# Kernel tuning notes

Measured on AMD Instinct MI355X. Metric: run time of the kernel, lower is better.

## Reference

```python
import jax, jax.numpy as jnp
import numpy as np

B_, N_, D_ = 8, 1024, 64
H_, DH_ = 4, 16
DI_, DS_, DTR_ = 128, 64, 4
MAXP = 512


def _ln(x, w, b, eps=1e-5):
    m = jnp.mean(x, -1, keepdims=True)
    v = jnp.mean((x - m) ** 2, -1, keepdims=True)
    return (x - m) * jax.lax.rsqrt(v + eps) * w + b


def _attn(x, drop_mask, Wq, Wkv, Wo, bo, rel_emb):
    b, n, d = x.shape
    scale = DH_ ** -0.5
    q = (x @ Wq).reshape(b, n, H_, DH_).transpose(0, 2, 1, 3)
    kv = x @ Wkv
    k = kv[..., :d].reshape(b, n, H_, DH_).transpose(0, 2, 1, 3)
    v = kv[..., d:].reshape(b, n, H_, DH_).transpose(0, 2, 1, 3)
    dots = jnp.einsum('bhid,bhjd->bhij', q, k) * scale
    seq = jnp.arange(n)
    dist = jnp.clip(seq[:, None] - seq[None, :], -MAXP, MAXP) + MAXP
    rpe = rel_emb[dist]  # (n, n, DH_)
    dots = dots + jnp.einsum('bhid,ijd->bhij', q, rpe) * scale
    # stochastic key drop: Bernoulli(0.3) positions get -1e12
    dots = dots + drop_mask.astype(dots.dtype) * (-1e12)
    attn = jax.nn.softmax(dots, axis=-1)
    out = jnp.einsum('bhij,bhjd->bhid', attn, v)
    out = out.transpose(0, 2, 1, 3).reshape(b, n, H_ * DH_)
    return out @ Wo + bo


def _mamba(x, W_in, conv_w, conv_b, W_xproj, W_dt, b_dt, A_log, Dm, W_out):
    b, n, _ = x.shape
    xz = x @ W_in                      # (b, n, 2*DI_)
    u, z = xz[..., :DI_], xz[..., DI_:]
    uc = u.transpose(0, 2, 1)          # (b, DI_, n)
    uc = jax.lax.conv_general_dilated(
        uc, conv_w[:, None, :], (1,), ((3, 0),),
        feature_group_count=DI_, dimension_numbers=('NCH', 'OIH', 'NCH'))
    uc = uc + conv_b[None, :, None]
    u = jax.nn.silu(uc).transpose(0, 2, 1)  # (b, n, DI_)
    xdb = u @ W_xproj                  # (b, n, DTR_+2*DS_)
    dt = jax.nn.softplus(xdb[..., :DTR_] @ W_dt + b_dt)  # (b, n, DI_)
    Bm = xdb[..., DTR_:DTR_ + DS_]
    Cm = xdb[..., DTR_ + DS_:]
    A = -jnp.exp(A_log)                # (DI_, DS_)

    def step(h, inp):
        dt_t, B_t, C_t, u_t = inp      # (b,DI_),(b,DS_),(b,DS_),(b,DI_)
        dA = jnp.exp(dt_t[..., None] * A)
        h = h * dA + (dt_t * u_t)[..., None] * B_t[:, None, :]
        y = jnp.einsum('bds,bs->bd', h, C_t)
        return h, y

    h0 = jnp.zeros((b, DI_, DS_), x.dtype)
    xs = (dt.transpose(1, 0, 2), Bm.transpose(1, 0, 2),
          Cm.transpose(1, 0, 2), u.transpose(1, 0, 2))
    _, ys = jax.lax.scan(step, h0, xs)
    y = ys.transpose(1, 0, 2) + u * Dm
    y = y * jax.nn.silu(z)
    return y @ W_out


def _rmsgn(x, gamma, eps=1e-5, groups=4):
    shp = x.shape
    dpg = shp[-1] // groups
    xg = x.reshape(shp[:-1] + (groups, dpg))
    rms = jnp.sqrt(jnp.sum(xg * xg, -1, keepdims=True)) * (dpg ** -0.5)
    return (xg / (rms + eps)).reshape(shp) * gamma


def _ff1(x, c1_w, c1_b, d1_w, d1_b):
    # SwiGLUConvDeconv1d(64, 256, kernel=4, shift=1); x: (b, s2, 64)
    s2 = x.shape[1]
    xc = x.transpose(0, 2, 1)
    xc = jnp.pad(xc, ((0, 0), (0, 0), (3, 3)))
    xc = jax.lax.conv_general_dilated(
        xc, c1_w, (1,), 'VALID', dimension_numbers=('NCH', 'OIH', 'NCH'))
    xc = xc + c1_b[None, :, None]
    gate = jax.nn.silu(xc[:, 256:, :])
    xc = xc[:, :256, :] * gate
    # ConvTranspose1d stride 1 == conv with flipped kernel, full padding
    w = jnp.flip(d1_w, -1).transpose(1, 0, 2)  # (64, 256, 4)
    xc = jax.lax.conv_general_dilated(
        xc, w, (1,), ((3, 3),), dimension_numbers=('NCH', 'OIH', 'NCH'))
    xc = xc + d1_b[None, :, None]
    out = xc.transpose(0, 2, 1)
    return out[:, 3:3 + s2, :]


def _forward(x, drop_mask, ln1_w, ln1_b, Wq, Wkv, Wo, bo, rel_emb,
             ln2_w, ln2_b, W_in, conv_w, conv_b, W_xproj, W_dt, b_dt,
             A_log, Dm, W_out, gamma, c1_w, c1_b, d1_w, d1_b, ln3_w, ln3_b):
    xt = _ln(x, ln1_w, ln1_b)
    xt = _attn(xt, drop_mask, Wq, Wkv, Wo, bo, rel_emb) + x
    x = x + xt  # dropout p=0 -> identity (faithful to original residual math)
    xt = _ln(x, ln2_w, ln2_b)
    m = _mamba(xt, W_in, conv_w, conv_b, W_xproj, W_dt, b_dt, A_log, Dm, W_out)
    m = jnp.where(m >= 0, m, 0.01 * m)  # leaky_relu
    m = _rmsgn(m, gamma)
    m = m + 0.5 * _ff1(m, c1_w, c1_b, d1_w, d1_b)
    x = x + m
    return _ln(x, ln3_w, ln3_b)


def setup_inputs() -> dict:
    ks = jax.random.split(jax.random.key(0), 16)
    g = lambda i, shp, s: jax.random.normal(ks[i], shp, dtype=jnp.float32) * s
    A_log = jnp.log(jnp.tile(jnp.arange(1, DS_ + 1, dtype=jnp.float32)[None, :], (DI_, 1)))
    return {
        'x': jax.random.normal(ks[0], (B_, N_, D_), dtype=jnp.float32),
        'drop_mask': jax.random.bernoulli(ks[1], 0.3, (B_, H_, N_, N_)),
        'ln1_w': jnp.ones((D_,), jnp.float32), 'ln1_b': jnp.zeros((D_,), jnp.float32),
        'Wq': g(2, (D_, D_), 0.1), 'Wkv': g(3, (D_, 2 * D_), 0.1),
        'Wo': g(4, (D_, D_), 0.1), 'bo': jnp.zeros((D_,), jnp.float32),
        'rel_emb': g(5, (2 * MAXP + 1, DH_), 0.02),
        'ln2_w': jnp.ones((D_,), jnp.float32), 'ln2_b': jnp.zeros((D_,), jnp.float32),
        'W_in': g(6, (D_, 2 * DI_), 0.1),
        'conv_w': g(7, (DI_, 4), 0.2), 'conv_b': jnp.zeros((DI_,), jnp.float32),
        'W_xproj': g(8, (DI_, DTR_ + 2 * DS_), 0.1),
        'W_dt': g(9, (DTR_, DI_), 0.1), 'b_dt': jnp.zeros((DI_,), jnp.float32),
        'A_log': A_log, 'Dm': jnp.ones((DI_,), jnp.float32),
        'W_out': g(10, (DI_, D_), 0.1),
        'gamma': jnp.ones((D_,), jnp.float32),
        'c1_w': g(11, (512, 64, 4), 0.1), 'c1_b': jnp.zeros((512,), jnp.float32),
        'd1_w': g(12, (256, 64, 4), 0.1), 'd1_b': jnp.zeros((64,), jnp.float32),
        'ln3_w': jnp.ones((D_,), jnp.float32), 'ln3_b': jnp.zeros((D_,), jnp.float32),
    }


def reference(x, drop_mask, ln1_w, ln1_b, Wq, Wkv, Wo, bo, rel_emb,
              ln2_w, ln2_b, W_in, conv_w, conv_b, W_xproj, W_dt, b_dt,
              A_log, Dm, W_out, gamma, c1_w, c1_b, d1_w, d1_b, ln3_w, ln3_b):
    return _forward(x, drop_mask, ln1_w, ln1_b, Wq, Wkv, Wo, bo, rel_emb,
                    ln2_w, ln2_b, W_in, conv_w, conv_b, W_xproj, W_dt, b_dt,
                    A_log, Dm, W_out, gamma, c1_w, c1_b, d1_w, d1_b, ln3_w, ln3_b)
```

## Files before the change

kernel.cpp:

```cpp
#include <hip/hip_runtime.h>
#include <math.h>


__device__ __forceinline__ float wsum64(float v){
#pragma unroll
  for(int m=32;m>0;m>>=1) v += __shfl_xor(v, m, 64);
  return v;
}
__device__ __forceinline__ float wmax64(float v){
#pragma unroll
  for(int m=32;m>0;m>>=1) v = fmaxf(v, __shfl_xor(v, m, 64));
  return v;
}
__device__ __forceinline__ float silu_f(float x){ return x / (1.f + __expf(-x)); }

__global__ __launch_bounds__(256) void k_ln1_qkv(
    const float* __restrict__ x, const float* __restrict__ w1, const float* __restrict__ b1,
    const float* __restrict__ Wq, const float* __restrict__ Wkv,
    const float* __restrict__ rel, const float* __restrict__ c1w,
    float* __restrict__ qb, float2* __restrict__ kvT,
    float* __restrict__ relT, float* __restrict__ c1wT){
  int lane = threadIdx.x & 63, warp = threadIdx.x >> 6;
  int token = blockIdx.x*4 + warp;
  __shared__ float xt[4][64];
  float xv = x[(size_t)token*64 + lane];
  float mean = wsum64(xv) * 0.015625f;
  float dlt = xv - mean;
  float var = wsum64(dlt*dlt) * 0.015625f;
  float xn = dlt * rsqrtf(var + 1e-5f) * w1[lane] + b1[lane];
  xt[warp][lane] = xn;
  __syncthreads();
  float aq=0.f, ak=0.f, av=0.f;
#pragma unroll 4
  for(int dd=0; dd<64; ++dd){
    float xd = xt[warp][dd];
    aq += xd * Wq[dd*64 + lane];
    ak += xd * Wkv[dd*128 + lane];
    av += xd * Wkv[dd*128 + 64 + lane];
  }
  int b = token >> 10, i = token & 1023;
  int h = lane >> 4, dh = lane & 15;
  size_t o  = (((size_t)(b*4 + h))*1024 + i)*16 + dh;
  size_t oT = (((size_t)(b*4 + h))*16 + dh)*1024 + i;
  qb[o]=aq;
  kvT[oT] = make_float2(ak, av);

  if (blockIdx.x < 65){
    int idx = blockIdx.x*256 + threadIdx.x;
    if (idx < 16*1025){
      int c = idx / 1025;
      int d = idx - c*1025;
      relT[idx] = rel[d*16 + c];
    }
  } else if (blockIdx.x < 577){
    int idx = (blockIdx.x-65)*256 + threadIdx.x;
    int row = idx >> 9;
    int ii  = idx & 511;
    c1wT[idx] = c1w[(size_t)ii*256 + row];
  }
}

__global__ __launch_bounds__(256) void k_kmax(
    const float2* __restrict__ kvT, float* __restrict__ Kmax){
  int bh = blockIdx.x; int tid = threadIdx.x;
  const float2* base = kvT + (size_t)bh*16*1024;
  float mx = 0.f;
#pragma unroll
  for(int r=0;r<4;++r){
    int j = tid + 256*r;
    float ss = 0.f;
#pragma unroll
    for(int c=0;c<16;++c){ float2 kv = base[c*1024 + j]; ss += kv.x*kv.x; }
    mx = fmaxf(mx, ss);
  }
  mx = wmax64(mx);
  __shared__ float red[4];
  int lane = tid&63, wv = tid>>6;
  if(lane==0) red[wv]=mx;
  __syncthreads();
  if(tid==0) Kmax[bh] = sqrtf(fmaxf(fmaxf(red[0],red[1]),fmaxf(red[2],red[3])));
}

__global__ __launch_bounds__(256, 3) void k_attn(
    const float* __restrict__ qb, const float2* __restrict__ kvT,
    const int* __restrict__ dmask, const float* __restrict__ relT,
    const float* __restrict__ Kmax, float* __restrict__ attn_raw){
  int tid = threadIdx.x;
  int lane = tid & 63, wv = tid >> 6;
  int bh  = blockIdx.y;
  int i0  = blockIdx.x*8;
  int b = bh >> 2, h = bh & 3;
  int r0 = wv*2, r1 = wv*2 + 1;

  __shared__ float Gc[8][1024];
  __shared__ float qs[8][16];
  __shared__ float G0s[8], G1024s[8];
  __shared__ float gmS[8];
  __shared__ float Ms[8];
  __shared__ float sums[8];

  if (tid < 128){
    int r = tid >> 4, c = tid & 15;
    qs[r][c] = qb[((size_t)bh*1024 + i0 + r)*16 + c] * 0.25f;
  }
  __syncthreads();

#pragma unroll 1
  for(int bb=0; bb<5; ++bb){
    int d = tid + 256*bb;
    if (d <= 1024){
      float rl[16];
#pragma unroll
      for(int c=0;c<16;++c) rl[c] = relT[c*1025 + d];
#pragma unroll
      for(int r=0;r<8;++r){
        float g = 0.f;
#pragma unroll
        for(int c=0;c<16;++c) g += qs[r][c]*rl[c];
        if (d == 0)        G0s[r] = g;
        else if (d == 1024) G1024s[r] = g;
        else {
          int j = i0 + r + 512 - d;
          if (j >= 0 && j < 1024) Gc[r][j] = g;
        }
      }
    }
  }
  __syncthreads();
#pragma unroll
  for(int r=0;r<8;++r){
    float g0 = G0s[r], g1 = G1024s[r];
    int lo = i0 + r - 512;
    int hi = i0 + r + 512;
#pragma unroll
    for(int p=0;p<4;++p){
      int j = tid + 256*p;
      if (j >= hi) Gc[r][j] = g0;
      else if (j <= lo) Gc[r][j] = g1;
    }
  }
  __syncthreads();
  {
    int r = tid >> 5, jb = tid & 31;
    float gm = -3.0e38f;
#pragma unroll
    for(int k=0;k<32;++k) gm = fmaxf(gm, Gc[r][jb + 32*k]);
#pragma unroll
    for(int m=1;m<32;m<<=1) gm = fmaxf(gm, __shfl_xor(gm, m, 64));
    if ((lane&31)==0) gmS[r] = gm;
  }
  __syncthreads();
  if (tid < 8){
    float qn = 0.f;
#pragma unroll
    for(int c=0;c<16;++c) qn += qs[tid][c]*qs[tid][c];
    Ms[tid] = gmS[tid] + sqrtf(qn)*Kmax[bh];
  }
  __syncthreads();

  float q0[16], q1[16];
#pragma unroll
  for(int c=0;c<16;++c){ q0[c]=qs[r0][c]; q1[c]=qs[r1][c]; }
  float M0 = Ms[r0], M1 = Ms[r1];

  const float2* kvb = kvT + (size_t)bh*16*1024;
  const int* mb0 = dmask + ((size_t)bh*1024 + i0 + r0)*1024;
  const int* mb1 = dmask + ((size_t)bh*1024 + i0 + r1)*1024;

  float s0=0.f, s1=0.f;
  float a0[16], a1[16];
#pragma unroll
  for(int c=0;c<16;++c){ a0[c]=0.f; a1[c]=0.f; }

#pragma unroll 1
  for(int t=0;t<16;++t){
    int j = lane + 64*t;
    int mk0 = mb0[j], mk1 = mb1[j];
    float2 kv[16];
#pragma unroll
    for(int c=0;c<16;++c) kv[c] = kvb[c*1024 + j];
    float sv0 = Gc[r0][j], sv1 = Gc[r1][j];
#pragma unroll
    for(int c=0;c<16;++c){ sv0 += q0[c]*kv[c].x; sv1 += q1[c]*kv[c].x; }
    float p0 = mk0 ? 0.f : __expf(sv0 - M0);
    float p1 = mk1 ? 0.f : __expf(sv1 - M1);
    s0 += p0; s1 += p1;
#pragma unroll
    for(int c=0;c<16;++c){ a0[c] += p0*kv[c].y; a1[c] += p1*kv[c].y; }
  }
  s0 = wsum64(s0); s1 = wsum64(s1);
#pragma unroll
  for(int c=0;c<16;++c){
    float x0 = a0[c];
    x0 += __shfl_xor(x0, 32, 64); x0 += __shfl_xor(x0, 16, 64);
    a0[c] = x0;
    float x1 = a1[c];
    x1 += __shfl_xor(x1, 32, 64); x1 += __shfl_xor(x1, 16, 64);
    a1[c] = x1;
  }
  __syncthreads();
  float* red = &Gc[0][0];
  if (lane < 16){
#pragma unroll
    for(int c=0;c<16;++c){
      red[r0*272 + lane*17 + c] = a0[c];
      red[r1*272 + lane*17 + c] = a1[c];
    }
  }
  if (lane == 0){ sums[r0] = s0; sums[r1] = s1; }
  __syncthreads();
  if (tid < 128){
    int row = tid >> 4, c = tid & 15;
    float tot = 0.f;
#pragma unroll
    for(int g=0; g<16; ++g) tot += red[row*272 + g*17 + c];
    attn_raw[((size_t)b*1024 + i0 + row)*64 + h*16 + c] = tot / sums[row];
  }
}

__global__ __launch_bounds__(256) void k_post_attn(
    const float* __restrict__ x, const float* __restrict__ attn_raw,
    const float* __restrict__ Wo, const float* __restrict__ bo,
    const float* __restrict__ ln2w, const float* __restrict__ ln2b,
    const float* __restrict__ W_in,
    float* __restrict__ x2, float* __restrict__ u0, float* __restrict__ zsarr){
  int tid = threadIdx.x;
  int lane = tid & 63, wv = tid >> 6;
  int tok0 = blockIdx.x * 16;
  __shared__ float arS[16][64];
  __shared__ float lnS[16][64];
  for(int l = tid; l < 1024; l += 256)
    arS[l >> 6][l & 63] = attn_raw[(size_t)tok0*64 + l];
  __syncthreads();
#pragma unroll 1
  for(int tt = 0; tt < 4; ++tt){
    int tl = wv*4 + tt;
    int token = tok0 + tl;
    float acc = bo[lane];
#pragma unroll 4
    for(int dd = 0; dd < 64; ++dd) acc += arS[tl][dd] * Wo[dd*64 + lane];
    float t = 2.f*x[(size_t)token*64 + lane] + acc;
    x2[(size_t)token*64 + lane] = t;
    float mean = wsum64(t)*0.015625f;
    float dlt = t - mean;
    float var = wsum64(dlt*dlt)*0.015625f;
    lnS[tl][lane] = dlt*rsqrtf(var+1e-5f)*ln2w[lane] + ln2b[lane];
  }
  __syncthreads();
  int oc = tid;
  float w[64];
#pragma unroll
  for(int dd = 0; dd < 64; ++dd) w[dd] = W_in[dd*256 + oc];
  const float4* lnS4 = (const float4*)&lnS[0][0];
#pragma unroll 1
  for(int tl = 0; tl < 16; ++tl){
    float acc = 0.f;
#pragma unroll
    for(int d4 = 0; d4 < 16; ++d4){
      float4 l4 = lnS4[tl*16 + d4];
      acc += l4.x*w[4*d4] + l4.y*w[4*d4+1] + l4.z*w[4*d4+2] + l4.w*w[4*d4+3];
    }
    int token = tok0 + tl;
    if (oc < 128) u0[(size_t)token*128 + oc] = acc;
    else          zsarr[(size_t)token*128 + (oc-128)] = silu_f(acc);
  }
}

__global__ __launch_bounds__(256) void k_conv_proj(
    const float* __restrict__ u0, const float* __restrict__ conv_w, const float* __restrict__ conv_b,
    const float* __restrict__ W_xproj, const float* __restrict__ W_dt, const float* __restrict__ b_dt,
    float* __restrict__ uarr, float* __restrict__ Bmp, float* __restrict__ Cmp, float* __restrict__ dtarr){
  int sub = threadIdx.x >> 7, c = threadIdx.x & 127;
  int token = blockIdx.x*2 + sub;
  int b = token >> 10, i = token & 1023;
  __shared__ float us[2][128];
  __shared__ float dtin[2][4];
  float acc = conv_b[c];
#pragma unroll
  for(int k2=0;k2<4;++k2){
    int t2 = i - 3 + k2;
    if (t2 >= 0) acc += u0[((size_t)b*1024 + t2)*128 + c]*conv_w[c*4+k2];
  }
  float uv = silu_f(acc);
  uarr[(size_t)token*128 + c] = uv;
  us[sub][c] = uv;
  __syncthreads();
  float accA = 0.f, accB = 0.f;
  int cB = 128 + (c & 3);
#pragma unroll 4
  for(int dd=0; dd<128; ++dd){
    float xd = us[sub][dd];
    accA += xd * W_xproj[dd*132 + c];
    accB += xd * W_xproj[dd*132 + cB];
  }
  if (c < 4){ dtin[sub][c] = accA; Cmp[(size_t)token*64 + 60 + c] = accB; }
  else if (c < 68) Bmp[(size_t)token*64 + (c-4)] = accA;
  else             Cmp[(size_t)token*64 + (c-68)] = accA;
  __syncthreads();
  float dv = b_dt[c];
#pragma unroll
  for(int r2=0;r2<4;++r2) dv += dtin[sub][r2]*W_dt[r2*128 + c];
  dv = fmaxf(dv, 0.f) + log1pf(expf(-fabsf(dv)));
  dtarr[(size_t)token*128 + c] = dv;
}

__global__ __launch_bounds__(256) void k_scan_a(
    const float* __restrict__ dtarr, const float* __restrict__ uarr,
    const float* __restrict__ Bmp, const float* __restrict__ A_log,
    float* __restrict__ Parr, float* __restrict__ Rarr){
  int lane = threadIdx.x & 63, warp = threadIdx.x >> 6;
  int w = blockIdx.x*4 + warp;
  int c = w & 7, d = (w >> 3) & 127, b = w >> 10;
  float A = -expf(A_log[d*64 + lane]);
  int tb = c*128;
  const float* dtp = dtarr + ((size_t)b*1024 + tb)*128 + d;
  const float* up  = uarr  + ((size_t)b*1024 + tb)*128 + d;
  const float* Bp  = Bmp   + ((size_t)b*1024 + tb)*64 + lane;
  float R = 0.f, sdt = 0.f;
  for(int t0=0; t0<128; t0+=8){
    float dtc[8], uc[8], Bc[8];
#pragma unroll
    for(int r=0;r<8;++r){
      dtc[r]=dtp[(size_t)(t0+r)*128]; uc[r]=up[(size_t)(t0+r)*128]; Bc[r]=Bp[(size_t)(t0+r)*64];
    }
#pragma unroll
    for(int r=0;r<8;++r){
      float dt = dtc[r];
      R = R*__expf(dt*A) + dt*uc[r]*Bc[r];
      sdt += dt;
    }
  }
  Parr[(size_t)w*64 + lane] = __expf(sdt*A);
  Rarr[(size_t)w*64 + lane] = R;
}

__global__ __launch_bounds__(256) void k_scan_c(
    const float* __restrict__ dtarr, const float* __restrict__ uarr,
    const float* __restrict__ Bmp, const float* __restrict__ Cmp,
    const float* __restrict__ zsarr, const float* __restrict__ A_log,
    const float* __restrict__ Dm, const float* __restrict__ Parr,
    const float* __restrict__ Rarr, float* __restrict__ ymp){
  int lane = threadIdx.x & 63, warp = threadIdx.x >> 6;
  int w = blockIdx.x*4 + warp;
  int c = w & 7, d = (w >> 3) & 127, b = w >> 10;
  float A = -expf(A_log[d*64 + lane]);
  float Dv = Dm[d];
  float h = 0.f;
  int wbase = w - c;
#pragma unroll 1
  for(int cp=0; cp<c; ++cp){
    float P = Parr[(size_t)(wbase+cp)*64 + lane];
    float R = Rarr[(size_t)(wbase+cp)*64 + lane];
    h = h*P + R;
  }
  int tb = c*128;
  const float* dtp = dtarr + ((size_t)b*1024 + tb)*128 + d;
  const float* up  = uarr  + ((size_t)b*1024 + tb)*128 + d;
  const float* zp  = zsarr + ((size_t)b*1024 + tb)*128 + d;
  const float* Bp  = Bmp   + ((size_t)b*1024 + tb)*64 + lane;
  const float* Cp  = Cmp   + ((size_t)b*1024 + tb)*64 + lane;
  float* yp        = ymp   + ((size_t)b*1024 + tb)*128 + d;
  for(int t0=0; t0<128; t0+=8){
    float dtc[8], uc[8], Bc[8], Cc[8], zc[8];
#pragma unroll
    for(int r=0;r<8;++r){
      dtc[r]=dtp[(size_t)(t0+r)*128]; uc[r]=up[(size_t)(t0+r)*128];
      Bc[r]=Bp[(size_t)(t0+r)*64];    Cc[r]=Cp[(size_t)(t0+r)*64];
      zc[r]=zp[(size_t)(t0+r)*128];
    }
    float hc[8];
#pragma unroll
    for(int r=0;r<8;++r){
      float dt = dtc[r];
      h = h*__expf(dt*A) + dt*uc[r]*Bc[r];
      hc[r] = h*Cc[r];
    }
    float y[8];
#pragma unroll
    for(int r=0;r<8;++r) y[r] = wsum64(hc[r]);
    if (lane==0){
#pragma unroll
      for(int r=0;r<8;++r) yp[(size_t)(t0+r)*128] = (y[r] + uc[r]*Dv)*zc[r];
    }
  }
}

__global__ __launch_bounds__(256) void k_wout(
    const float* __restrict__ ymp, const float* __restrict__ W_out,
    const float* __restrict__ gamma, float* __restrict__ marr){
  int lane = threadIdx.x & 63, warp = threadIdx.x >> 6;
  int token = blockIdx.x*4 + warp;
  __shared__ float ys[4][128];
  ys[warp][lane]      = ymp[(size_t)token*128 + lane];
  ys[warp][lane+64]   = ymp[(size_t)token*128 + 64 + lane];
  __syncthreads();
  float acc = 0.f;
#pragma unroll 4
  for(int dd=0; dd<128; ++dd) acc += ys[warp][dd]*W_out[dd*64 + lane];
  acc = acc >= 0.f ? acc : 0.01f*acc;
  float ss = acc*acc;
#pragma unroll
  for(int m=1;m<16;m<<=1) ss += __shfl_xor(ss, m, 64);
  float rms = sqrtf(ss)*0.25f;
  marr[(size_t)token*64 + lane] = acc/(rms + 1e-5f)*gamma[lane];
}

__global__ __launch_bounds__(256) void k_h2(
    const float* __restrict__ marr, const float* __restrict__ c1wT,
    const float* __restrict__ c1b, float* __restrict__ h2){
  int b = blockIdx.y;
  int t0 = blockIdx.x * 16;
  int tid = threadIdx.x;
  __shared__ float ms[19][64];
  for(int l = tid; l < 19*64; l += 256){
    int row = l >> 6, cc = l & 63;
    int t = t0 - 3 + row;
    ms[row][cc] = (t >= 0 && t < 1024) ? marr[((size_t)b*1024 + t)*64 + cc] : 0.f;
  }
  __syncthreads();
  int i = tid;
  float acc1[16], acc2[16];
#pragma unroll
  for(int tl=0;tl<16;++tl){ acc1[tl]=0.f; acc2[tl]=0.f; }
  for(int cc=0; cc<64; ++cc){
    float mv[19];
#pragma unroll
    for(int r2=0;r2<19;++r2) mv[r2] = ms[r2][cc];
    const float* wr = c1wT + (size_t)cc*4*512;
    float wa0 = wr[      i], wa1 = wr[ 512+i], wa2 = wr[1024+i], wa3 = wr[1536+i];
    float wg0 = wr[  256+i], wg1 = wr[ 768+i], wg2 = wr[1280+i], wg3 = wr[1792+i];
#pragma unroll
    for(int tl=0; tl<16; ++tl){
      acc1[tl] += wa0*mv[tl+0] + wa1*mv[tl+1] + wa2*mv[tl+2] + wa3*mv[tl+3];
      acc2[tl] += wg0*mv[tl+0] + wg1*mv[tl+1] + wg2*mv[tl+2] + wg3*mv[tl+3];
    }
  }
  float bb1 = c1b[i], bb2 = c1b[i+256];
#pragma unroll
  for(int tl=0; tl<16; ++tl){
    int t = t0 + tl;
    if (t < 1027){
      float o1 = acc1[tl] + bb1;
      float o2 = acc2[tl] + bb2;
      h2[((size_t)b*1027 + t)*256 + i] = o1 * silu_f(o2);
    }
  }
}

__global__ __launch_bounds__(256) void k_ff_final(
    const float* __restrict__ h2, const float* __restrict__ d1w, const float* __restrict__ d1b,
    const float* __restrict__ x2, const float* __restrict__ marr,
    const float* __restrict__ ln3w, const float* __restrict__ ln3b,
    float* __restrict__ out){
  int b = blockIdx.y;
  int s0 = blockIdx.x * 16;
  int tid = threadIdx.x;
  int o = tid & 63, sg = tid >> 6;
  __shared__ float hs[19][256];
  for(int l = tid; l < 19*256; l += 256){
    int row = l >> 8, cc = l & 255;
    hs[row][cc] = h2[((size_t)b*1027 + s0 + row)*256 + cc];
  }
  __syncthreads();
  int sl = sg*4;
  float acc0=0.f, acc1=0.f, acc2=0.f, acc3=0.f;
  const float4* wb = (const float4*)d1w + o;
#pragma unroll 2
  for(int i2=0; i2<256; ++i2){
    float4 wv = wb[(size_t)i2*64];
    float h0=hs[sl+0][i2], h1=hs[sl+1][i2], h2v=hs[sl+2][i2], h3=hs[sl+3][i2];
    float h4=hs[sl+4][i2], h5=hs[sl+5][i2], h6=hs[sl+6][i2];
    acc0 += h0*wv.w + h1*wv.z + h2v*wv.y + h3*wv.x;
    acc1 += h1*wv.w + h2v*wv.z + h3*wv.y + h4*wv.x;
    acc2 += h2v*wv.w + h3*wv.z + h4*wv.y + h5*wv.x;
    acc3 += h3*wv.w + h4*wv.z + h5*wv.y + h6*wv.x;
  }
  float accs[4] = {acc0, acc1, acc2, acc3};
  float bo_ = d1b[o];
#pragma unroll
  for(int r=0;r<4;++r){
    int s = s0 + sl + r;
    size_t idx = ((size_t)b*1024 + s)*64 + o;
    float tot = x2[idx] + marr[idx] + 0.5f*(accs[r] + bo_);
    float mean = wsum64(tot)*0.015625f;
    float dlt = tot - mean;
    float var = wsum64(dlt*dlt)*0.015625f;
    out[idx] = dlt*rsqrtf(var+1e-5f)*ln3w[o] + ln3b[o];
  }
}

extern "C" void kernel_launch(void* const* d_in, const int* in_sizes, int n_in,
                              void* d_out, int out_size, void* d_ws, size_t ws_size,
                              hipStream_t stream){
  const float* x       = (const float*)d_in[0];
  const int*   dmask   = (const int*)  d_in[1];
  const float* ln1w    = (const float*)d_in[2];
  const float* ln1b    = (const float*)d_in[3];
  const float* Wq      = (const float*)d_in[4];
  const float* Wkv     = (const float*)d_in[5];
  const float* Wo      = (const float*)d_in[6];
  const float* bo      = (const float*)d_in[7];
  const float* rel     = (const float*)d_in[8];
  const float* ln2w    = (const float*)d_in[9];
  const float* ln2b    = (const float*)d_in[10];
  const float* W_in    = (const float*)d_in[11];
  const float* conv_w  = (const float*)d_in[12];
  const float* conv_b  = (const float*)d_in[13];
  const float* W_xproj = (const float*)d_in[14];
  const float* W_dt    = (const float*)d_in[15];
  const float* b_dt    = (const float*)d_in[16];
  const float* A_log   = (const float*)d_in[17];
  const float* Dm      = (const float*)d_in[18];
  const float* W_out   = (const float*)d_in[19];
  const float* gamma   = (const float*)d_in[20];
  const float* c1w     = (const float*)d_in[21];
  const float* c1b     = (const float*)d_in[22];
  const float* d1w     = (const float*)d_in[23];
  const float* d1b     = (const float*)d_in[24];
  const float* ln3w    = (const float*)d_in[25];
  const float* ln3b    = (const float*)d_in[26];
  float* outp = (float*)d_out;

  float* ws = (float*)d_ws;
  float* qb       = ws;
  float* kvT      = qb      + 524288;
  float* attn_raw = kvT     + 1048576;
  float* x2       = attn_raw+ 524288;
  float* u0       = x2      + 524288;
  float* zsarr    = u0      + 1048576;
  float* uarr     = zsarr   + 1048576;
  float* dtarr    = uarr    + 1048576;
  float* Bmp      = dtarr   + 1048576;
  float* Cmp      = Bmp     + 524288;
  float* ymp      = Cmp     + 524288;
  float* marr     = ymp     + 1048576;
  float* h2       = marr    + 524288;
  float* relT     = h2      + 2103296;
  float* c1wT     = relT    + 16400;
  float* Parr     = c1wT    + 131072;
  float* Rarr     = Parr    + 524288;
  float* Kmaxa    = Rarr    + 524288;

  k_ln1_qkv  <<<2048, 256, 0, stream>>>(x, ln1w, ln1b, Wq, Wkv, rel, c1w,
                                        qb, (float2*)kvT, relT, c1wT);
  k_kmax     <<<32, 256, 0, stream>>>((const float2*)kvT, Kmaxa);
  k_attn     <<<dim3(128,32), 256, 0, stream>>>(qb, (const float2*)kvT, dmask, relT, Kmaxa, attn_raw);
  k_post_attn<<<512, 256, 0, stream>>>(x, attn_raw, Wo, bo, ln2w, ln2b, W_in, x2, u0, zsarr);
  k_conv_proj<<<4096, 256, 0, stream>>>(u0, conv_w, conv_b, W_xproj, W_dt, b_dt, uarr, Bmp, Cmp, dtarr);
  k_scan_a   <<<2048, 256, 0, stream>>>(dtarr, uarr, Bmp, A_log, Parr, Rarr);
  k_scan_c   <<<2048, 256, 0, stream>>>(dtarr, uarr, Bmp, Cmp, zsarr, A_log, Dm, Parr, Rarr, ymp);
  k_wout     <<<2048, 256, 0, stream>>>(ymp, W_out, gamma, marr);
  k_h2       <<<dim3(65,8), 256, 0, stream>>>(marr, c1wT, c1b, h2);
  k_ff_final <<<dim3(64,8), 256, 0, stream>>>(h2, d1w, d1b, x2, marr, ln3w, ln3b, outp);
}
```

Before: 736.1 us.

## Pack drop mask into bitmask and fold it into precomputed score bias

The int32 drop mask is packed into 64-bit ballot words inside the Kmax kernel, using spare blocks. The attention kernel reads those bits when it builds the relative-position bias rows and writes -1e30 for dropped keys, so the inner loop no longer loads the per-element int mask or branches on it. The mask buffer reuses the later h2 scratch area. The attention launch bound rises to 4 blocks per SM, which may increase register pressure or spills.

Result: slower. 818.4 us (+11.2%).

```diff
diff --git a/kernel.cpp b/kernel.cpp
--- a/kernel.cpp
+++ b/kernel.cpp
@@ -60,9 +60,23 @@
   }
 }
 
-__global__ __launch_bounds__(256) void k_kmax(
-    const float2* __restrict__ kvT, float* __restrict__ Kmax){
-  int bh = blockIdx.x; int tid = threadIdx.x;
+__global__ __launch_bounds__(256) void k_kmax_pack(
+    const float2* __restrict__ kvT, float* __restrict__ Kmax,
+    const int* __restrict__ dmask, unsigned long long* __restrict__ mask64){
+  int tid = threadIdx.x;
+  if (blockIdx.x >= 32){
+    size_t base = (size_t)(blockIdx.x - 32) * 16384;
+    const int* dp = dmask + base;
+    unsigned long long* mp = mask64 + (base >> 6);
+#pragma unroll 4
+    for(int r=0;r<64;++r){
+      int m = dp[r*256 + tid];
+      unsigned long long bal = __ballot(m != 0);
+      if ((tid & 63) == 0) mp[r*4 + (tid >> 6)] = bal;
+    }
+    return;
+  }
+  int bh = blockIdx.x;
   const float2* base = kvT + (size_t)bh*16*1024;
   float mx = 0.f;
 #pragma unroll
@@ -81,9 +95,9 @@
   if(tid==0) Kmax[bh] = sqrtf(fmaxf(fmaxf(red[0],red[1]),fmaxf(red[2],red[3])));
 }
 
-__global__ __launch_bounds__(256, 3) void k_attn(
+__global__ __launch_bounds__(256, 4) void k_attn(
     const float* __restrict__ qb, const float2* __restrict__ kvT,
-    const int* __restrict__ dmask, const float* __restrict__ relT,
+    const unsigned long long* __restrict__ mask64, const float* __restrict__ relT,
     const float* __restrict__ Kmax, float* __restrict__ attn_raw){
   int tid = threadIdx.x;
   int lane = tid & 63, wv = tid >> 6;
@@ -127,16 +141,24 @@
     }
   }
   __syncthreads();
-#pragma unroll
-  for(int r=0;r<8;++r){
-    float g0 = G0s[r], g1 = G1024s[r];
-    int lo = i0 + r - 512;
-    int hi = i0 + r + 512;
-#pragma unroll
-    for(int p=0;p<4;++p){
-      int j = tid + 256*p;
-      if (j >= hi) Gc[r][j] = g0;
-      else if (j <= lo) Gc[r][j] = g1;
+  {
+    const unsigned long long* mrow = mask64 + ((size_t)bh*1024 + i0)*16;
+#pragma unroll
+    for(int r=0;r<8;++r){
+      float g0 = G0s[r], g1 = G1024s[r];
+      int lo = i0 + r - 512;
+      int hi = i0 + r + 512;
+#pragma unroll
+      for(int p=0;p<4;++p){
+        int j = tid + 256*p;
+        unsigned long long w = mrow[r*16 + (j>>6)];
+        float g;
+        if (j >= hi) g = g0;
+        else if (j <= lo) g = g1;
+        else g = Gc[r][j];
+        if ((w >> (j & 63)) & 1ULL) g = -1e30f;
+        Gc[r][j] = g;
+      }
     }
   }
   __syncthreads();
@@ -164,8 +186,6 @@
   float M0 = Ms[r0], M1 = Ms[r1];
 
   const float2* kvb = kvT + (size_t)bh*16*1024;
-  const int* mb0 = dmask + ((size_t)bh*1024 + i0 + r0)*1024;
-  const int* mb1 = dmask + ((size_t)bh*1024 + i0 + r1)*1024;
 
   float s0=0.f, s1=0.f;
   float a0[16], a1[16];
@@ -175,15 +195,14 @@
 #pragma unroll 1
   for(int t=0;t<16;++t){
     int j = lane + 64*t;
-    int mk0 = mb0[j], mk1 = mb1[j];
     float2 kv[16];
 #pragma unroll
     for(int c=0;c<16;++c) kv[c] = kvb[c*1024 + j];
     float sv0 = Gc[r0][j], sv1 = Gc[r1][j];
 #pragma unroll
     for(int c=0;c<16;++c){ sv0 += q0[c]*kv[c].x; sv1 += q1[c]*kv[c].x; }
-    float p0 = mk0 ? 0.f : __expf(sv0 - M0);
-    float p1 = mk1 ? 0.f : __expf(sv1 - M1);
+    float p0 = __expf(sv0 - M0);
+    float p1 = __expf(sv1 - M1);
     s0 += p0; s1 += p1;
 #pragma unroll
     for(int c=0;c<16;++c){ a0[c] += p0*kv[c].y; a1[c] += p1*kv[c].y; }
@@ -541,10 +560,12 @@
   float* Rarr     = Parr    + 524288;
   float* Kmaxa    = Rarr    + 524288;
 
+  unsigned long long* mask64 = (unsigned long long*)h2;
+
   k_ln1_qkv  <<<2048, 256, 0, stream>>>(x, ln1w, ln1b, Wq, Wkv, rel, c1w,
                                         qb, (float2*)kvT, relT, c1wT);
-  k_kmax     <<<32, 256, 0, stream>>>((const float2*)kvT, Kmaxa);
-  k_attn     <<<dim3(128,32), 256, 0, stream>>>(qb, (const float2*)kvT, dmask, relT, Kmaxa, attn_raw);
+  k_kmax_pack<<<2080, 256, 0, stream>>>((const float2*)kvT, Kmaxa, dmask, mask64);
+  k_attn     <<<dim3(128,32), 256, 0, stream>>>(qb, (const float2*)kvT, mask64, relT, Kmaxa, attn_raw);
   k_post_attn<<<512, 256, 0, stream>>>(x, attn_raw, Wo, bo, ln2w, ln2b, W_in, x2, u0, zsarr);
   k_conv_proj<<<4096, 256, 0, stream>>>(u0, conv_w, conv_b, W_xproj, W_dt, b_dt, uarr, Bmp, Cmp, dtarr);
   k_scan_a   <<<2048, 256, 0, stream>>>(dtarr, uarr, Bmp, A_log, Parr, Rarr);
```
